# Kernel tuning notes

Measured on AMD Instinct MI355X. Metric: run time of the kernel, lower is better.

Reference implementation:

```python
import jax, jax.numpy as jnp
import numpy as np
from math import factorial

NODES = 40000      # number of nodes
EDGES = 640000     # number of edges (avg degree 16)
MUL = 8            # multiplicity of each irrep in hidden (8x0e+8x1e+8x2e)
NB = 16            # radial basis size (radial_neurons[0])
MAXR = 3.0         # max_radius
NSPECIES = 8
DEG = 16.0         # num_neighbors normalization
R8 = 1.0 / np.sqrt(8.0)

# ---------- real Clebsch-Gordan coefficients (precomputed with numpy) ----------
def _clebsch(j1, m1, j2, m2, j3, m3):
    f = factorial
    if m1 + m2 != m3:
        return 0.0
    pref = ((2*j3+1) * f(j3+j1-j2) * f(j3-j1+j2) * f(j1+j2-j3) / f(j1+j2+j3+1)) ** 0.5
    pref *= (f(j3+m3)*f(j3-m3)*f(j1-m1)*f(j1+m1)*f(j2-m2)*f(j2+m2)) ** 0.5
    lo = max(0, j2-j3-m1, j1-j3+m2)
    hi = min(j1+j2-j3, j1-m1, j2+m2)
    s = 0.0
    for k in range(lo, hi+1):
        s += (-1)**k / (f(k)*f(j1+j2-j3-k)*f(j1-m1-k)*f(j2+m2-k)*f(j3-j2+m1+k)*f(j3-j1-m2+k))
    return pref * s

def _U(l):
    # complex -> real spherical-harmonic change of basis (rows: real m, cols: complex m)
    U = np.zeros((2*l+1, 2*l+1), dtype=complex)
    s2 = 2 ** -0.5
    for m in range(-l, l+1):
        if m > 0:
            U[m+l, m+l] = (-1)**m * s2; U[m+l, -m+l] = s2
        elif m == 0:
            U[l, l] = 1.0
        else:
            U[m+l, m+l] = 1j*s2; U[m+l, -m+l] = -1j*((-1)**m)*s2
    return U

def _real_cg(l1, l2, l3):
    C = np.zeros((2*l1+1, 2*l2+1, 2*l3+1))
    for m1 in range(-l1, l1+1):
        for m2 in range(-l2, l2+1):
            m3 = m1 + m2
            if abs(m3) <= l3:
                C[m1+l1, m2+l2, m3+l3] = _clebsch(l1, m1, l2, m2, l3, m3)
    T = np.einsum('am,bn,co,mno->abc', _U(l1).conj(), _U(l2).conj(), _U(l3), C)
    R = T.imag if np.abs(T.imag).max() > np.abs(T.real).max() else T.real
    return jnp.asarray(R.astype(np.float32))

PATHS = [(0,0,0),(0,1,1),(0,2,2),(1,0,1),(1,1,0),(1,1,1),(1,1,2),
         (1,2,1),(1,2,2),(2,0,2),(2,1,1),(2,1,2),(2,2,0),(2,2,1),(2,2,2)]
CG = {p: _real_cg(*p) for p in PATHS}
NIN = {0: 3.0, 1: 6.0, 2: 6.0}  # fan-in path counts per output l in hidden convs

# ---------- irrep feature layout: [.., 72] = 8x0e | 8x1e | 8x2e ----------
def _split(h):
    lead = h.shape[:-1]
    return (h[..., :MUL],
            h[..., MUL:4*MUL].reshape(lead + (MUL, 3)),
            h[..., 4*MUL:].reshape(lead + (MUL, 5)))

def _merge(s, v, t):
    lead = s.shape[:-1]
    return jnp.concatenate([s, v.reshape(lead + (3*MUL,)), t.reshape(lead + (5*MUL,))], -1)

def _act(h):
    # e3nn Activation: silu on 0e scalars, identity on l>0
    s, v, t = _split(h)
    return _merge(jax.nn.silu(s), v, t)

def _radial(emb, w1, b1, w2, b2):
    return jax.nn.silu(emb @ w1 + b1) @ w2 + b2

def _sh(u):
    # component-normalized real spherical harmonics l=0,1,2 of unit vectors u [E,3]
    x, y, z = u[:, 0], u[:, 1], u[:, 2]
    c15 = np.sqrt(15.0); c5 = np.sqrt(5.0); c3 = np.sqrt(3.0)
    y1 = jnp.stack([y, z, x], -1) * c3
    y2 = jnp.stack([c15*x*y, c15*y*z, 0.5*c5*(3*z*z - 1.0), c15*x*z, 0.5*c15*(x*x - y*y)], -1)
    return jnp.concatenate([jnp.ones_like(x)[:, None], y1, y2], -1)

def _soft_onehot(r):
    # e3nn soft_one_hot_linspace, basis='smooth_finite', cutoff=True
    values = jnp.linspace(0.0, MAXR, NB + 2)[1:-1]
    step = MAXR / (NB + 1)
    d = (r[:, None] - values) / step
    inside = jnp.abs(d) < 1.0
    dd = jnp.where(inside, d, 0.0)
    f = jnp.exp(-1.0 / (1.0 + dd)) * jnp.exp(-1.0 / (1.0 - dd))
    return 1.14136 * np.exp(2.0) * jnp.where(inside, f, 0.0)

def _tp_first(hs, sh, w):
    # uvu TP: 8x0e (x) SH(1x0e+1x1e+1x2e) -> hidden; hs [E,8], sh [E,9], w [E,3,8]
    m_s = w[:, 0] * hs * sh[:, :1]
    m_v = w[:, 1][..., None] * hs[..., None] * sh[:, None, 1:4]
    m_t = w[:, 2][..., None] * hs[..., None] * sh[:, None, 4:9]
    return _merge(m_s, m_v, m_t)

def _tp_uuu(h1, h2, w):
    # depthwise (uuu) CG tensor product hidden (x) hidden -> hidden; w [E,15,8]
    s1, v1, t1 = _split(h1); s2, v2, t2 = _split(h2)
    a = {0: s1[..., None], 1: v1, 2: t1}
    b = {0: s2[..., None], 1: v2, 2: t2}
    out = {0: 0.0, 1: 0.0, 2: 0.0}
    for p, (l1, l2, l3) in enumerate(PATHS):
        out[l3] = out[l3] + w[:, p, :, None] * jnp.einsum('eci,ecj,ijk->eck', a[l1], b[l2], CG[(l1, l2, l3)])
    return _merge(out[0][..., 0] / np.sqrt(NIN[0]), out[1] / np.sqrt(NIN[1]), out[2] / np.sqrt(NIN[2]))

def _lin_hidden(h, lin):
    # irrep-wise linear self-connection, lin [3,8,8]
    s, v, t = _split(h)
    return _merge(s @ lin[0] * R8,
                  jnp.einsum('ncm,cd->ndm', v, lin[1]) * R8,
                  jnp.einsum('ncm,cd->ndm', t, lin[2]) * R8)

def _model(x, edge_index, edge_vec, embed_w, lin0, lin1, lin2, out_w,
           r0_w1, r0_b1, r0_w2, r0_b2, r1_w1, r1_b1, r1_w2, r1_b2,
           r2_w1, r2_b1, r2_w2, r2_b2):
    src, dst = edge_index[0], edge_index[1]
    h = embed_w[x]                                   # [N, 8] scalar node feats
    r = jnp.sqrt(jnp.sum(edge_vec**2, -1) + 1e-12)
    emb = _soft_onehot(r)                            # [E, 16]
    hb_sh = _sh(edge_vec / r[:, None])               # [E, 9]
    rdeg = 1.0 / np.sqrt(DEG)
    # conv 0 + activation
    w = _radial(emb, r0_w1, r0_b1, r0_w2, r0_b2).reshape(-1, 3, MUL)
    m = _tp_first(h[src], hb_sh, w)                  # [E, 72]
    agg = jax.ops.segment_sum(m, dst, num_segments=NODES) * rdeg
    h = _act(agg.at[:, :MUL].add((h @ lin0) * R8))
    hb = _act(m)
    # convs 1..2 + activation
    for (w1, b1, w2, b2, lin) in ((r1_w1, r1_b1, r1_w2, r1_b2, lin1),
                                  (r2_w1, r2_b1, r2_w2, r2_b2, lin2)):
        w = _radial(emb, w1, b1, w2, b2).reshape(-1, 15, MUL)
        m = _tp_uuu(h[src], hb, w)
        agg = jax.ops.segment_sum(m, dst, num_segments=NODES) * rdeg
        h = _act(_lin_hidden(h, lin) + agg)
        hb = _act(m)
    # output FullyConnectedTensorProduct(h, h) -> 8x0e (paths l(x)l->0)
    s, v, t = _split(h)
    i0 = s[:, :, None] * s[:, None, :]
    i1 = jnp.einsum('nim,njm->nij', v, v) / np.sqrt(3.0)
    i2 = jnp.einsum('nim,njm->nij', t, t) / np.sqrt(5.0)
    out = (jnp.einsum('nij,ijk->nk', i0, out_w[0])
           + jnp.einsum('nij,ijk->nk', i1, out_w[1])
           + jnp.einsum('nij,ijk->nk', i2, out_w[2])) / np.sqrt(3.0 * MUL * MUL)
    return out

def setup_inputs() -> dict:
    key = jax.random.key(0)
    ks = jax.random.split(key, 16)
    inp = {}
    inp['x'] = jax.random.randint(ks[0], (NODES,), 0, NSPECIES)
    inp['edge_index'] = jax.random.randint(ks[1], (2, EDGES), 0, NODES)
    inp['edge_vec'] = jax.random.normal(ks[2], (EDGES, 3), dtype=jnp.float32)
    inp['embed_w'] = jax.random.normal(ks[3], (NSPECIES, MUL), dtype=jnp.float32)
    inp['lin0'] = jax.random.normal(ks[4], (MUL, MUL), dtype=jnp.float32)
    inp['lin1'] = jax.random.normal(ks[5], (3, MUL, MUL), dtype=jnp.float32)
    inp['lin2'] = jax.random.normal(ks[6], (3, MUL, MUL), dtype=jnp.float32)
    inp['out_w'] = jax.random.normal(ks[7], (3, MUL, MUL, MUL), dtype=jnp.float32)
    for i, (name, od) in enumerate((('r0', 3*MUL), ('r1', 15*MUL), ('r2', 15*MUL))):
        k1, k2 = jax.random.split(ks[8+i])
        inp[name+'_w1'] = jax.random.normal(k1, (NB, 64), dtype=jnp.float32) / np.sqrt(NB)
        inp[name+'_b1'] = jnp.zeros((64,), dtype=jnp.float32)
        inp[name+'_w2'] = jax.random.normal(k2, (64, od), dtype=jnp.float32) / 8.0
        inp[name+'_b2'] = jnp.zeros((od,), dtype=jnp.float32)
    return inp

def reference(x, edge_index, edge_vec, embed_w, lin0, lin1, lin2, out_w,
              r0_w1, r0_b1, r0_w2, r0_b2, r1_w1, r1_b1, r1_w2, r1_b2,
              r2_w1, r2_b1, r2_w2, r2_b2):
    return _model(x, edge_index, edge_vec, embed_w, lin0, lin1, lin2, out_w,
                  r0_w1, r0_b1, r0_w2, r0_b2, r1_w1, r1_b1, r1_w2, r1_b2,
                  r2_w1, r2_b1, r2_w2, r2_b2)
```

## Files before the change

kernel.cpp:

```cpp
#include <hip/hip_runtime.h>

#define NODES 40000
#define EDGES 640000

typedef float f32x2v __attribute__((ext_vector_type(2)));
typedef float f32x4v __attribute__((ext_vector_type(4)));
typedef short short8v __attribute__((ext_vector_type(8)));

__device__ __forceinline__ float silu_f(float x) { return x / (1.0f + __expf(-x)); }
__device__ __forceinline__ f32x2v mk2(float a, float b) { f32x2v r; r[0] = a; r[1] = b; return r; }

__device__ __forceinline__ void tp_uuu2(const f32x2v* wv,
                                        f32x2v as, const f32x2v* av, const f32x2v* at,
                                        f32x2v bs, const f32x2v* bv, const f32x2v* bt,
                                        f32x2v& ms, f32x2v* mv, f32x2v* mt)
{
    const float CR = 0.70710678f;
    const float K1 = 0.31622777f;
    const float K3 = 0.54772256f;
    const float KA = 0.40824829f;
    const float KB = 0.70710678f;
    const float KC = 0.81649658f;
    const float L4 = 0.63245553f;
    const float G2 = 0.53452248f;
    const float G1 = 0.26726124f;
    const float HH = 0.46291005f;

    f32x2v os = {0.f, 0.f};
    f32x2v ov0 = {0.f, 0.f}, ov1 = {0.f, 0.f}, ov2 = {0.f, 0.f};
    f32x2v ot0 = {0.f, 0.f}, ot1 = {0.f, 0.f}, ot2 = {0.f, 0.f};
    f32x2v ot3 = {0.f, 0.f}, ot4 = {0.f, 0.f};

    os += wv[0] * as * bs;
    ov0 += wv[1] * as * bv[0]; ov1 += wv[1] * as * bv[1]; ov2 += wv[1] * as * bv[2];
    ot0 += wv[2] * as * bt[0]; ot1 += wv[2] * as * bt[1]; ot2 += wv[2] * as * bt[2];
    ot3 += wv[2] * as * bt[3]; ot4 += wv[2] * as * bt[4];
    ov0 += wv[3] * av[0] * bs; ov1 += wv[3] * av[1] * bs; ov2 += wv[3] * av[2] * bs;
    os += wv[4] * (-0.57735027f) * (av[0]*bv[0] + av[1]*bv[1] + av[2]*bv[2]);
    ov0 += wv[5] * CR * (av[1]*bv[2] - av[2]*bv[1]);
    ov1 += wv[5] * CR * (av[2]*bv[0] - av[0]*bv[2]);
    ov2 += wv[5] * CR * (av[0]*bv[1] - av[1]*bv[0]);
    ot0 += wv[6] * CR * (av[2]*bv[0] + av[0]*bv[2]);
    ot1 += wv[6] * CR * (av[0]*bv[1] + av[1]*bv[0]);
    ot2 += wv[6] * 0.40824829f * (2.f*av[1]*bv[1] - av[2]*bv[2] - av[0]*bv[0]);
    ot3 += wv[6] * CR * (av[2]*bv[1] + av[1]*bv[2]);
    ot4 += wv[6] * CR * (av[2]*bv[2] - av[0]*bv[0]);
    ov0 += wv[7] * (-K3*av[1]*bt[1] + K1*av[0]*bt[2] - K3*av[2]*bt[0] + K3*av[0]*bt[4]);
    ov1 += wv[7] * (-2.f*K1*av[1]*bt[2] - K3*av[2]*bt[3] - K3*av[0]*bt[1]);
    ov2 += wv[7] * (-K3*av[1]*bt[3] + K1*av[2]*bt[2] - K3*av[0]*bt[0] - K3*av[2]*bt[4]);
    ot0 += wv[8] * ( KC*av[1]*bt[4] - KA*av[2]*bt[3] + KA*av[0]*bt[1]);
    ot1 += wv[8] * ( KA*av[1]*bt[3] - KB*av[2]*bt[2] - KA*av[0]*bt[0] - KA*av[2]*bt[4]);
    ot2 += wv[8] * ( KB*av[2]*bt[1] - KB*av[0]*bt[3]);
    ot3 += wv[8] * (-KA*av[1]*bt[1] + KB*av[0]*bt[2] + KA*av[2]*bt[0] - KA*av[0]*bt[4]);
    ot4 += wv[8] * (-KC*av[1]*bt[0] + KA*av[2]*bt[1] + KA*av[0]*bt[3]);
    ot0 += wv[9] * at[0] * bs; ot1 += wv[9] * at[1] * bs; ot2 += wv[9] * at[2] * bs;
    ot3 += wv[9] * at[3] * bs; ot4 += wv[9] * at[4] * bs;
    ov0 += wv[10] * (-K3*bv[1]*at[1] + K1*bv[0]*at[2] - K3*bv[2]*at[0] + K3*bv[0]*at[4]);
    ov1 += wv[10] * (-2.f*K1*bv[1]*at[2] - K3*bv[2]*at[3] - K3*bv[0]*at[1]);
    ov2 += wv[10] * (-K3*bv[1]*at[3] + K1*bv[2]*at[2] - K3*bv[0]*at[0] - K3*bv[2]*at[4]);
    ot0 -= wv[11] * ( KC*bv[1]*at[4] - KA*bv[2]*at[3] + KA*bv[0]*at[1]);
    ot1 -= wv[11] * ( KA*bv[1]*at[3] - KB*bv[2]*at[2] - KA*bv[0]*at[0] - KA*bv[2]*at[4]);
    ot2 -= wv[11] * ( KB*bv[2]*at[1] - KB*bv[0]*at[3]);
    ot3 -= wv[11] * (-KA*bv[1]*at[1] + KB*bv[0]*at[2] + KA*bv[2]*at[0] - KA*bv[0]*at[4]);
    ot4 -= wv[11] * (-KC*bv[1]*at[0] + KA*bv[2]*at[1] + KA*bv[0]*at[3]);
    os += wv[12] * 0.44721360f * (at[0]*bt[0] + at[1]*bt[1] + at[2]*bt[2] + at[3]*bt[3] + at[4]*bt[4]);
    ov0 += wv[13] * ( K1*(at[0]*bt[1] - at[1]*bt[0]) + K3*(at[3]*bt[2] - at[2]*bt[3]) + K1*(at[4]*bt[3] - at[3]*bt[4]) );
    ov1 += wv[13] * ( L4*(at[0]*bt[4] - at[4]*bt[0]) + K1*(at[1]*bt[3] - at[3]*bt[1]) );
    ov2 += wv[13] * ( K1*(at[3]*bt[0] - at[0]*bt[3]) + K3*(at[2]*bt[1] - at[1]*bt[2]) + K1*(at[4]*bt[1] - at[1]*bt[4]) );
    ot0 += wv[14] * ( G2*(at[2]*bt[0] + at[0]*bt[2]) - HH*(at[1]*bt[3] + at[3]*bt[1]) );
    ot1 += wv[14] * (-HH*(at[3]*bt[0] + at[0]*bt[3]) + HH*(at[1]*bt[4] + at[4]*bt[1]) - G1*(at[2]*bt[1] + at[1]*bt[2]) );
    ot2 += wv[14] * ( G2*(at[0]*bt[0] + at[4]*bt[4] - at[2]*bt[2]) - G1*(at[1]*bt[1] + at[3]*bt[3]) );
    ot3 += wv[14] * (-HH*(at[1]*bt[0] + at[0]*bt[1]) - HH*(at[3]*bt[4] + at[4]*bt[3]) - G1*(at[2]*bt[3] + at[3]*bt[2]) );
    ot4 += wv[14] * ( G2*(at[2]*bt[4] + at[4]*bt[2]) + HH*(at[1]*bt[1] - at[3]*bt[3]) );

    ms = os * 0.57735027f;
    mv[0] = ov0 * 0.40824829f; mv[1] = ov1 * 0.40824829f; mv[2] = ov2 * 0.40824829f;
    mt[0] = ot0 * 0.40824829f; mt[1] = ot1 * 0.40824829f; mt[2] = ot2 * 0.40824829f;
    mt[3] = ot3 * 0.40824829f; mt[4] = ot4 * 0.40824829f;
}

__global__ void deg_kernel(const int* __restrict__ eidx, int* __restrict__ deg)
{
    int e = blockIdx.x * 256 + threadIdx.x;
    if (e < EDGES) atomicAdd(&deg[eidx[EDGES + e]], 1);
}

__launch_bounds__(1024)
__global__ void scan_kernel(const int* __restrict__ deg, int* __restrict__ off,
                            int* __restrict__ cursor)
{
    __shared__ int part[1024];
    const int t = threadIdx.x;
    const int base = t * 40;
    int v[40];
    if (t < 1000) {
        const int4* p4 = (const int4*)(deg + base);
        #pragma unroll
        for (int i = 0; i < 10; ++i) {
            int4 q = p4[i];
            v[4 * i + 0] = q.x; v[4 * i + 1] = q.y;
            v[4 * i + 2] = q.z; v[4 * i + 3] = q.w;
        }
    } else {
        #pragma unroll
        for (int i = 0; i < 40; ++i) v[i] = 0;
    }
    int loc[40];
    int s = 0;
    #pragma unroll
    for (int i = 0; i < 40; ++i) { loc[i] = s; s += v[i]; }
    part[t] = s;
    __syncthreads();
    for (int d = 1; d < 1024; d <<= 1) {
        int vv = (t >= d) ? part[t - d] : 0;
        __syncthreads();
        part[t] += vv;
        __syncthreads();
    }
    int tb = (t == 0) ? 0 : part[t - 1];
    if (t < 1000) {
        #pragma unroll
        for (int i = 0; i < 40; ++i) {
            off[base + i] = tb + loc[i];
            cursor[base + i] = tb + loc[i];
        }
    }
    if (t == 1023) off[NODES] = part[1023];
}

__global__ void build_kernel(const int* __restrict__ eidx, const float* __restrict__ ev,
                             int* __restrict__ cursor,
                             float* __restrict__ evp, int* __restrict__ srcs)
{
    int e = blockIdx.x * 256 + threadIdx.x;
    if (e < EDGES) {
        int dst = eidx[EDGES + e];
        int p = atomicAdd(&cursor[dst], 1);
        srcs[p] = eidx[e];
        evp[p * 3 + 0] = ev[e * 3 + 0];
        evp[p * 3 + 1] = ev[e * 3 + 1];
        evp[p * 3 + 2] = ev[e * 3 + 2];
    }
}

__launch_bounds__(256, 3)
__global__ void layer0_edge(const float* __restrict__ evp, const int* __restrict__ srcs,
                            const int* __restrict__ xs, const float* __restrict__ embw,
                            const float* __restrict__ w1, const float* __restrict__ b1,
                            const float* __restrict__ w2, const float* __restrict__ b2,
                            float* __restrict__ mbuf)
{
    __shared__ float emb_s[128 * 17];
    __shared__ float hid_s[128 * 68];
    __shared__ float w2t[24 * 68];
    const int tid = threadIdx.x;
    const int e0 = blockIdx.x * 128;

    for (int idx = tid; idx < 64 * 24; idx += 256) {
        int j = idx / 24, o = idx - j * 24;
        w2t[o * 68 + j] = w2[idx];
    }
    for (int idx = tid; idx < 2048; idx += 256) {
        int e = idx >> 4, i = idx & 15;
        const float* ep = evp + (size_t)(e0 + e) * 3;
        float ex = ep[0], ey = ep[1], ez = ep[2];
        float r = sqrtf(ex * ex + ey * ey + ez * ez + 1e-12f);
        float d = r * (17.0f / 3.0f) - (float)(i + 1);
        float f = 0.0f;
        if (fabsf(d) < 1.0f) f = 8.433572869f * __expf(-2.0f / (1.0f - d * d));
        emb_s[e * 17 + i] = f;
    }
    __syncthreads();

    {
        const int egp = tid >> 3;
        const int jb = (tid & 7) * 8;
        float acc2[4][8];
        #pragma unroll
        for (int el = 0; el < 4; ++el)
            #pragma unroll
            for (int k = 0; k < 8; ++k) acc2[el][k] = b1[jb + k];
        #pragma unroll
        for (int i = 0; i < 16; ++i) {
            float4 wa = *(const float4*)&w1[i * 64 + jb];
            float4 wb = *(const float4*)&w1[i * 64 + jb + 4];
            #pragma unroll
            for (int el = 0; el < 4; ++el) {
                float evv = emb_s[(egp * 4 + el) * 17 + i];
                acc2[el][0] += evv * wa.x; acc2[el][1] += evv * wa.y;
                acc2[el][2] += evv * wa.z; acc2[el][3] += evv * wa.w;
                acc2[el][4] += evv * wb.x; acc2[el][5] += evv * wb.y;
                acc2[el][6] += evv * wb.z; acc2[el][7] += evv * wb.w;
            }
        }
        #pragma unroll
        for (int el = 0; el < 4; ++el)
            #pragma unroll
            for (int k = 0; k < 8; ++k)
                hid_s[(egp * 4 + el) * 68 + jb + k] = silu_f(acc2[el][k]);
    }
    __syncthreads();

    const int c = tid & 7, g = (tid >> 3) & 7, wv_ = tid >> 6;
    float wacc[3][4];
    #pragma unroll
    for (int p = 0; p < 3; ++p) {
        float bb = b2[p * 8 + c];
        #pragma unroll
        for (int q = 0; q < 4; ++q) wacc[p][q] = bb;
    }
    for (int jb = 0; jb < 64; jb += 4) {
        float4 h4[4];
        #pragma unroll
        for (int q = 0; q < 4; ++q)
            h4[q] = *(const float4*)&hid_s[(wv_ * 32 + q * 8 + g) * 68 + jb];
        #pragma unroll
        for (int p = 0; p < 3; ++p) {
            float4 w4 = *(const float4*)&w2t[(p * 8 + c) * 68 + jb];
            #pragma unroll
            for (int q = 0; q < 4; ++q)
                wacc[p][q] += h4[q].x * w4.x + h4[q].y * w4.y + h4[q].z * w4.z + h4[q].w * w4.w;
        }
    }

    const int ebase = wv_ * 32 + g;
    const float c3 = 1.7320508f, c15 = 3.8729833f, c5 = 2.2360680f;
    #pragma unroll
    for (int q = 0; q < 4; ++q) {
        const int sl = e0 + ebase + 8 * q;
        const int sn = srcs[sl];
        float hs = embw[xs[sn] * 8 + c];
        const float* ep = evp + (size_t)sl * 3;
        float ex = ep[0], ey = ep[1], ez = ep[2];
        float r = sqrtf(ex * ex + ey * ey + ez * ez + 1e-12f);
        float inv = 1.0f / r;
        float x = ex * inv, y = ey * inv, z = ez * inv;

        float* me = mbuf + (size_t)sl * 72 + c * 9;
        me[0] = wacc[0][q] * hs;
        me[1] = wacc[1][q] * hs * (c3 * y);
        me[2] = wacc[1][q] * hs * (c3 * z);
        me[3] = wacc[1][q] * hs * (c3 * x);
        me[4] = wacc[2][q] * hs * (c15 * x * y);
        me[5] = wacc[2][q] * hs * (c15 * y * z);
        me[6] = wacc[2][q] * hs * (0.5f * c5 * (3.f * z * z - 1.f));
        me[7] = wacc[2][q] * hs * (c15 * x * z);
        me[8] = wacc[2][q] * hs * (0.5f * c15 * (x * x - y * y));
    }
}

__launch_bounds__(256, 3)
__global__ void tp_edge(const float* __restrict__ evp, const int* __restrict__ srcs,
                        const float* __restrict__ h,
                        const float* __restrict__ w1, const float* __restrict__ b1,
                        const float* __restrict__ w2, const float* __restrict__ b2,
                        float* __restrict__ mbuf)
{
    __shared__ float ws_t[120 * 68];
    __shared__ unsigned short hid_s[128 * 64];
    float* emb_s = ws_t;

    const int tid = threadIdx.x;
    const int e0 = blockIdx.x * 128;

    for (int idx = tid; idx < 2048; idx += 256) {
        int e = idx >> 4, i = idx & 15;
        const float* ep = evp + (size_t)(e0 + e) * 3;
        float ex = ep[0], ey = ep[1], ez = ep[2];
        float r = sqrtf(ex * ex + ey * ey + ez * ez + 1e-12f);
        float d = r * (17.0f / 3.0f) - (float)(i + 1);
        float f = 0.0f;
        if (fabsf(d) < 1.0f) f = 8.433572869f * __expf(-2.0f / (1.0f - d * d));
        emb_s[e * 17 + i] = f;
    }
    __syncthreads();

    {
        const int egp = tid >> 3;
        const int jb = (tid & 7) * 8;
        f32x2v acc2[2][8];
        #pragma unroll
        for (int pr = 0; pr < 2; ++pr)
            #pragma unroll
            for (int k = 0; k < 8; ++k) { float bb = b1[jb + k]; acc2[pr][k] = mk2(bb, bb); }
        #pragma unroll
        for (int i = 0; i < 16; ++i) {
            float4 wa = *(const float4*)&w1[i * 64 + jb];
            float4 wb = *(const float4*)&w1[i * 64 + jb + 4];
            #pragma unroll
            for (int pr = 0; pr < 2; ++pr) {
                f32x2v evv = mk2(emb_s[(egp * 4 + 2 * pr) * 17 + i],
                                 emb_s[(egp * 4 + 2 * pr + 1) * 17 + i]);
                acc2[pr][0] += evv * wa.x; acc2[pr][1] += evv * wa.y;
                acc2[pr][2] += evv * wa.z; acc2[pr][3] += evv * wa.w;
                acc2[pr][4] += evv * wb.x; acc2[pr][5] += evv * wb.y;
                acc2[pr][6] += evv * wb.z; acc2[pr][7] += evv * wb.w;
            }
        }
        #pragma unroll
        for (int pr = 0; pr < 2; ++pr) {
            #pragma unroll
            for (int u = 0; u < 2; ++u) {
                unsigned int us[8];
                #pragma unroll
                for (int k = 0; k < 8; ++k) {
                    unsigned int b = __float_as_uint(silu_f(acc2[pr][k][u]));
                    b += 0x7fffu + ((b >> 16) & 1u);
                    us[k] = b >> 16;
                }
                uint4 pk;
                pk.x = us[0] | (us[1] << 16);
                pk.y = us[2] | (us[3] << 16);
                pk.z = us[4] | (us[5] << 16);
                pk.w = us[6] | (us[7] << 16);
                int rr = egp * 4 + 2 * pr + u;
                *(uint4*)&hid_s[rr * 64 + (jb ^ ((rr & 7) << 3))] = pk;
            }
        }
    }
    __syncthreads();

    const int l  = tid & 63;
    const int wq = tid >> 6;
    const int lr = l & 15;
    const int lg = l >> 4;

    short8v bhi[2][2], blo[2][2];
    #pragma unroll
    for (int n2 = 0; n2 < 2; ++n2) {
        int col  = (2 * wq + n2) * 16 + lr;
        int colc = col < 120 ? col : 119;
        #pragma unroll
        for (int ks = 0; ks < 2; ++ks) {
            short8v hv, lv;
            #pragma unroll
            for (int j = 0; j < 8; ++j) {
                int k = ks * 32 + lg * 8 + j;
                float v = w2[k * 120 + colc];
                if (col >= 120) v = 0.0f;
                unsigned bb = __float_as_uint(v);
                unsigned rh = bb + 0x7fffu + ((bb >> 16) & 1u);
                float hf = __uint_as_float((rh >> 16) << 16);
                unsigned bl = __float_as_uint(v - hf);
                bl += 0x7fffu + ((bl >> 16) & 1u);
                hv[j] = (short)(rh >> 16);
                lv[j] = (short)(bl >> 16);
            }
            bhi[n2][ks] = hv;
            blo[n2][ks] = lv;
        }
    }

    const int c = tid & 7, g = (tid >> 3) & 7, wv_ = tid >> 6;
    const int ebh = wv_ * 16 + g;

    #pragma unroll
    for (int half = 0; half < 2; ++half) {
        #pragma unroll
        for (int mm = 0; mm < 4; ++mm) {
            int e  = 64 * half + 16 * mm + lr;
            int sw = (e & 7) << 3;
            short8v a0 = *(const short8v*)&hid_s[e * 64 + ((lg * 8) ^ sw)];
            short8v a1 = *(const short8v*)&hid_s[e * 64 + ((32 + lg * 8) ^ sw)];
            #pragma unroll
            for (int n2 = 0; n2 < 2; ++n2) {
                int col = (2 * wq + n2) * 16 + lr;
                float bias = (col < 120) ? b2[col] : 0.0f;
                f32x4v acc;
                acc[0] = bias; acc[1] = bias; acc[2] = bias; acc[3] = bias;
                acc = __builtin_amdgcn_mfma_f32_16x16x32_bf16(a0, bhi[n2][0], acc, 0, 0, 0);
                acc = __builtin_amdgcn_mfma_f32_16x16x32_bf16(a1, bhi[n2][1], acc, 0, 0, 0);
                acc = __builtin_amdgcn_mfma_f32_16x16x32_bf16(a0, blo[n2][0], acc, 0, 0, 0);
                acc = __builtin_amdgcn_mfma_f32_16x16x32_bf16(a1, blo[n2][1], acc, 0, 0, 0);
                if (col < 120)
                    *(f32x4v*)&ws_t[col * 68 + 16 * mm + lg * 4] = acc;
            }
        }
        __syncthreads();

        {
            const int eA = e0 + 64 * half + ebh;
            const int eB = eA + 8;
            const int snA = srcs[eA], snB = srcs[eB];
            const float* hn0 = h + (size_t)snA * 72 + c * 9;
            const float* hn1 = h + (size_t)snB * 72 + c * 9;
            const float* me0 = mbuf + (size_t)eA * 72 + c * 9;
            const float* me1 = mbuf + (size_t)eB * 72 + c * 9;

            f32x2v as = mk2(hn0[0], hn1[0]);
            f32x2v av[3], at[5], bv[3], bt[5];
            #pragma unroll
            for (int i = 0; i < 3; ++i) av[i] = mk2(hn0[1 + i], hn1[1 + i]);
            #pragma unroll
            for (int i = 0; i < 5; ++i) at[i] = mk2(hn0[4 + i], hn1[4 + i]);
            f32x2v bs = mk2(silu_f(me0[0]), silu_f(me1[0]));
            #pragma unroll
            for (int i = 0; i < 3; ++i) bv[i] = mk2(me0[1 + i], me1[1 + i]);
            #pragma unroll
            for (int i = 0; i < 5; ++i) bt[i] = mk2(me0[4 + i], me1[4 + i]);

            f32x2v wvv[15];
            #pragma unroll
            for (int p = 0; p < 15; ++p)
                wvv[p] = mk2(ws_t[(p * 8 + c) * 68 + ebh],
                             ws_t[(p * 8 + c) * 68 + ebh + 8]);

            f32x2v ms, mv[3], mt[5];
            tp_uuu2(wvv, as, av, at, bs, bv, bt, ms, mv, mt);

            float* mo0 = mbuf + (size_t)eA * 72 + c * 9;
            float* mo1 = mbuf + (size_t)eB * 72 + c * 9;
            mo0[0] = ms[0]; mo1[0] = ms[1];
            #pragma unroll
            for (int i = 0; i < 3; ++i) { mo0[1 + i] = mv[i][0]; mo1[1 + i] = mv[i][1]; }
            #pragma unroll
            for (int i = 0; i < 5; ++i) { mo0[4 + i] = mt[i][0]; mo1[4 + i] = mt[i][1]; }
        }
        if (half == 0) __syncthreads();
    }
}

__global__ void node0(const int* __restrict__ xs, const float* __restrict__ embw,
                      const float* __restrict__ lin0, const float* __restrict__ mbuf,
                      const int* __restrict__ off, float* __restrict__ h)
{
    int idx = blockIdx.x * 256 + threadIdx.x;
    int n = idx >> 3, c = idx & 7;
    int xb = xs[n] * 8;
    float dot = 0.f;
    #pragma unroll
    for (int d = 0; d < 8; ++d) dot += embw[xb + d] * lin0[d * 8 + c];

    float an[9];
    #pragma unroll
    for (int i = 0; i < 9; ++i) an[i] = 0.f;
    const int beg = off[n], end = off[n + 1];
    for (int p = beg; p < end; ++p) {
        const float* me = mbuf + (size_t)p * 72 + c * 9;
        #pragma unroll
        for (int i = 0; i < 9; ++i) an[i] += me[i];
    }

    float* hn = h + (size_t)n * 72 + c * 9;
    hn[0] = silu_f(an[0] * 0.25f + dot * 0.35355339f);
    #pragma unroll
    for (int i = 1; i < 9; ++i) hn[i] = an[i] * 0.25f;
}

__global__ void node12(const float* __restrict__ hin, const float* __restrict__ lin,
                       const float* __restrict__ mbuf, const int* __restrict__ off,
                       float* __restrict__ hout)
{
    int idx = blockIdx.x * 256 + threadIdx.x;
    int n = idx >> 3, d = idx & 7;

    float an[9];
    #pragma unroll
    for (int i = 0; i < 9; ++i) an[i] = 0.f;
    const int beg = off[n], end = off[n + 1];
    for (int p = beg; p < end; ++p) {
        const float* me = mbuf + (size_t)p * 72 + d * 9;
        #pragma unroll
        for (int i = 0; i < 9; ++i) an[i] += me[i];
    }

    const float* hn = hin + (size_t)n * 72;
    float* ho = hout + (size_t)n * 72 + d * 9;

    float s = 0.f;
    #pragma unroll
    for (int c = 0; c < 8; ++c) s += hn[c * 9] * lin[c * 8 + d];
    ho[0] = silu_f(s * 0.35355339f + an[0] * 0.25f);
    #pragma unroll
    for (int i = 0; i < 3; ++i) {
        float v = 0.f;
        #pragma unroll
        for (int c = 0; c < 8; ++c) v += hn[c * 9 + 1 + i] * lin[64 + c * 8 + d];
        ho[1 + i] = v * 0.35355339f + an[1 + i] * 0.25f;
    }
    #pragma unroll
    for (int i = 0; i < 5; ++i) {
        float t = 0.f;
        #pragma unroll
        for (int c = 0; c < 8; ++c) t += hn[c * 9 + 4 + i] * lin[128 + c * 8 + d];
        ho[4 + i] = t * 0.35355339f + an[4 + i] * 0.25f;
    }
}

__global__ void node12_out(const float* __restrict__ hin, const float* __restrict__ lin,
                           const float* __restrict__ mbuf, const int* __restrict__ off,
                           const float* __restrict__ outw, float* __restrict__ out)
{
    __shared__ float hrec[32][72];
    int idx = blockIdx.x * 256 + threadIdx.x;
    int n = idx >> 3, d = idx & 7;
    int nl = threadIdx.x >> 3;

    float an[9];
    #pragma unroll
    for (int i = 0; i < 9; ++i) an[i] = 0.f;
    const int beg = off[n], end = off[n + 1];
    for (int p = beg; p < end; ++p) {
        const float* me = mbuf + (size_t)p * 72 + d * 9;
        #pragma unroll
        for (int i = 0; i < 9; ++i) an[i] += me[i];
    }

    const float* hn = hin + (size_t)n * 72;
    float* ho = &hrec[nl][d * 9];

    float s = 0.f;
    #pragma unroll
    for (int c = 0; c < 8; ++c) s += hn[c * 9] * lin[c * 8 + d];
    ho[0] = silu_f(s * 0.35355339f + an[0] * 0.25f);
    #pragma unroll
    for (int i = 0; i < 3; ++i) {
        float v = 0.f;
        #pragma unroll
        for (int c = 0; c < 8; ++c) v += hn[c * 9 + 1 + i] * lin[64 + c * 8 + d];
        ho[1 + i] = v * 0.35355339f + an[1 + i] * 0.25f;
    }
    #pragma unroll
    for (int i = 0; i < 5; ++i) {
        float t = 0.f;
        #pragma unroll
        for (int c = 0; c < 8; ++c) t += hn[c * 9 + 4 + i] * lin[128 + c * 8 + d];
        ho[4 + i] = t * 0.35355339f + an[4 + i] * 0.25f;
    }
    __syncthreads();

    const float* hr = &hrec[nl][0];
    float sv[8], vv[24], tv[40];
    #pragma unroll
    for (int i = 0; i < 8; ++i) {
        sv[i] = hr[i * 9];
        #pragma unroll
        for (int q = 0; q < 3; ++q) vv[i * 3 + q] = hr[i * 9 + 1 + q];
        #pragma unroll
        for (int q = 0; q < 5; ++q) tv[i * 5 + q] = hr[i * 9 + 4 + q];
    }
    float acc = 0.f;
    #pragma unroll
    for (int i = 0; i < 8; ++i) {
        #pragma unroll
        for (int j = 0; j < 8; ++j) {
            float dv = vv[i*3+0]*vv[j*3+0] + vv[i*3+1]*vv[j*3+1] + vv[i*3+2]*vv[j*3+2];
            float dt = tv[i*5+0]*tv[j*5+0] + tv[i*5+1]*tv[j*5+1] + tv[i*5+2]*tv[j*5+2]
                     + tv[i*5+3]*tv[j*5+3] + tv[i*5+4]*tv[j*5+4];
            int o = (i * 8 + j) * 8 + d;
            acc += sv[i] * sv[j] * outw[o]
                 + dv * 0.57735027f * outw[512 + o]
                 + dt * 0.44721360f * outw[1024 + o];
        }
    }
    out[n * 8 + d] = acc * 0.072168784f;
}

extern "C" void kernel_launch(void* const* d_in, const int* in_sizes, int n_in,
                              void* d_out, int out_size, void* d_ws, size_t ws_size,
                              hipStream_t stream)
{
    const int*   x    = (const int*)  d_in[0];
    const int*   eidx = (const int*)  d_in[1];
    const float* ev   = (const float*)d_in[2];
    const float* embw = (const float*)d_in[3];
    const float* lin0 = (const float*)d_in[4];
    const float* lin1 = (const float*)d_in[5];
    const float* lin2 = (const float*)d_in[6];
    const float* outw = (const float*)d_in[7];
    const float* r0w1 = (const float*)d_in[8];
    const float* r0b1 = (const float*)d_in[9];
    const float* r0w2 = (const float*)d_in[10];
    const float* r0b2 = (const float*)d_in[11];
    const float* r1w1 = (const float*)d_in[12];
    const float* r1b1 = (const float*)d_in[13];
    const float* r1w2 = (const float*)d_in[14];
    const float* r1b2 = (const float*)d_in[15];
    const float* r2w1 = (const float*)d_in[16];
    const float* r2b1 = (const float*)d_in[17];
    const float* r2w2 = (const float*)d_in[18];
    const float* r2b2 = (const float*)d_in[19];

    float* mbuf = (float*)d_ws;
    float* hA   = mbuf + (size_t)EDGES * 72;
    float* hB   = hA + (size_t)NODES * 72;
    float* evp  = hB + (size_t)NODES * 72;
    int*   deg    = (int*)(evp + (size_t)EDGES * 3);
    int*   off    = deg + NODES;
    int*   cursor = off + NODES + 1;
    int*   srcs   = cursor + NODES;

    const int EBI = (EDGES + 255) / 256;
    const int EB  = EDGES / 128;
    const int NBK = NODES * 8 / 256;

    hipMemsetAsync(deg, 0, NODES * sizeof(int), stream);
    deg_kernel<<<EBI, 256, 0, stream>>>(eidx, deg);
    scan_kernel<<<1, 1024, 0, stream>>>(deg, off, cursor);
    build_kernel<<<EBI, 256, 0, stream>>>(eidx, ev, cursor, evp, srcs);

    layer0_edge<<<EB, 256, 0, stream>>>(evp, srcs, x, embw, r0w1, r0b1, r0w2, r0b2, mbuf);
    node0<<<NBK, 256, 0, stream>>>(x, embw, lin0, mbuf, off, hA);

    tp_edge<<<EB, 256, 0, stream>>>(evp, srcs, hA, r1w1, r1b1, r1w2, r1b2, mbuf);
    node12<<<NBK, 256, 0, stream>>>(hA, lin1, mbuf, off, hB);

    tp_edge<<<EB, 256, 0, stream>>>(evp, srcs, hB, r2w1, r2b1, r2w2, r2b2, mbuf);
    node12_out<<<NBK, 256, 0, stream>>>(hB, lin2, mbuf, off, outw, (float*)d_out);
}
```

Before: 680.7 us.

## Fuse segmented atomic aggregation into tp_edge and skip message store in last layer

Packs the destination node into the upper 16 bits of the CSR source array. This lets the tensor-product edge kernel stage each block's messages in shared memory and do a segmented reduction over runs of equal destinations, followed by atomicAdd into a per-node aggregate buffer. The node kernels then read the pre-summed aggregates instead of walking the large edge-message buffer. The last layer no longer writes messages at all. The cost is extra memsets, shared-memory syncs and float atomics, which make the summation order nondeterministic; the packing also relies on node ids fitting in 16 bits.

```diff
diff --git a/kernel.cpp b/kernel.cpp
--- a/kernel.cpp
+++ b/kernel.cpp
@@ -136,7 +136,7 @@
     if (e < EDGES) {
         int dst = eidx[EDGES + e];
         int p = atomicAdd(&cursor[dst], 1);
-        srcs[p] = eidx[e];
+        srcs[p] = (int)(((unsigned)eidx[e]) | ((unsigned)dst << 16));
         evp[p * 3 + 0] = ev[e * 3 + 0];
         evp[p * 3 + 1] = ev[e * 3 + 1];
         evp[p * 3 + 2] = ev[e * 3 + 2];
@@ -228,7 +228,7 @@
     #pragma unroll
     for (int q = 0; q < 4; ++q) {
         const int sl = e0 + ebase + 8 * q;
-        const int sn = srcs[sl];
+        const int sn = (int)((unsigned)srcs[sl] & 0xffffu);
         float hs = embw[xs[sn] * 8 + c];
         const float* ep = evp + (size_t)sl * 3;
         float ex = ep[0], ey = ep[1], ez = ep[2];
@@ -254,10 +254,12 @@
                         const float* __restrict__ h,
                         const float* __restrict__ w1, const float* __restrict__ b1,
                         const float* __restrict__ w2, const float* __restrict__ b2,
-                        float* __restrict__ mbuf)
+                        float* __restrict__ mbuf, float* __restrict__ agg,
+                        const int writeM)
 {
     __shared__ float ws_t[120 * 68];
     __shared__ unsigned short hid_s[128 * 64];
+    __shared__ int dst_s[66];
     float* emb_s = ws_t;
 
     const int tid = threadIdx.x;
@@ -381,7 +383,8 @@
         {
             const int eA = e0 + 64 * half + ebh;
             const int eB = eA + 8;
-            const int snA = srcs[eA], snB = srcs[eB];
+            const unsigned pkA = (unsigned)srcs[eA], pkB = (unsigned)srcs[eB];
+            const int snA = (int)(pkA & 0xffffu), snB = (int)(pkB & 0xffffu);
             const float* hn0 = h + (size_t)snA * 72 + c * 9;
             const float* hn1 = h + (size_t)snB * 72 + c * 9;
             const float* me0 = mbuf + (size_t)eA * 72 + c * 9;
@@ -408,13 +411,54 @@
             f32x2v ms, mv[3], mt[5];
             tp_uuu2(wvv, as, av, at, bs, bv, bt, ms, mv, mt);
 
-            float* mo0 = mbuf + (size_t)eA * 72 + c * 9;
-            float* mo1 = mbuf + (size_t)eB * 72 + c * 9;
-            mo0[0] = ms[0]; mo1[0] = ms[1];
-            #pragma unroll
-            for (int i = 0; i < 3; ++i) { mo0[1 + i] = mv[i][0]; mo1[1 + i] = mv[i][1]; }
-            #pragma unroll
-            for (int i = 0; i < 5; ++i) { mo0[4 + i] = mt[i][0]; mo1[4 + i] = mt[i][1]; }
+            if (writeM) {
+                float* mo0 = mbuf + (size_t)eA * 72 + c * 9;
+                float* mo1 = mbuf + (size_t)eB * 72 + c * 9;
+                mo0[0] = ms[0]; mo1[0] = ms[1];
+                #pragma unroll
+                for (int i = 0; i < 3; ++i) { mo0[1 + i] = mv[i][0]; mo1[1 + i] = mv[i][1]; }
+                #pragma unroll
+                for (int i = 0; i < 5; ++i) { mo0[4 + i] = mt[i][0]; mo1[4 + i] = mt[i][1]; }
+            }
+
+            if (tid <= 64) {
+                int gs = e0 + 64 * half + tid;
+                dst_s[tid] = (gs < EDGES) ? (int)((unsigned)srcs[gs] >> 16) : -1;
+            }
+            __syncthreads();
+
+            float* m_s = ws_t;
+            const int lA = ebh, lB = ebh + 8;
+            m_s[lA * 72 + c * 9] = ms[0]; m_s[lB * 72 + c * 9] = ms[1];
+            #pragma unroll
+            for (int i = 0; i < 3; ++i) {
+                m_s[lA * 72 + c * 9 + 1 + i] = mv[i][0];
+                m_s[lB * 72 + c * 9 + 1 + i] = mv[i][1];
+            }
+            #pragma unroll
+            for (int i = 0; i < 5; ++i) {
+                m_s[lA * 72 + c * 9 + 4 + i] = mt[i][0];
+                m_s[lB * 72 + c * 9 + 4 + i] = mt[i][1];
+            }
+            __syncthreads();
+
+            if (tid < 216) {
+                const int seg  = tid / 72;
+                const int comp = tid - seg * 72;
+                const int p0 = (seg == 0) ? 0  : ((seg == 1) ? 22 : 43);
+                const int p1 = (seg == 0) ? 22 : ((seg == 1) ? 43 : 64);
+                float sum = 0.f;
+                int cur = dst_s[p0];
+                for (int p = p0; p < p1; ++p) {
+                    sum += m_s[p * 72 + comp];
+                    int nxt = dst_s[p + 1];
+                    if (nxt != cur) {
+                        atomicAdd(&agg[(size_t)cur * 72 + comp], sum);
+                        sum = 0.f; cur = nxt;
+                    }
+                }
+                if (cur >= 0) atomicAdd(&agg[(size_t)cur * 72 + comp], sum);
+            }
         }
         if (half == 0) __syncthreads();
     }
@@ -448,21 +492,14 @@
 }
 
 __global__ void node12(const float* __restrict__ hin, const float* __restrict__ lin,
-                       const float* __restrict__ mbuf, const int* __restrict__ off,
-                       float* __restrict__ hout)
+                       const float* __restrict__ agg, float* __restrict__ hout)
 {
     int idx = blockIdx.x * 256 + threadIdx.x;
     int n = idx >> 3, d = idx & 7;
 
     float an[9];
     #pragma unroll
-    for (int i = 0; i < 9; ++i) an[i] = 0.f;
-    const int beg = off[n], end = off[n + 1];
-    for (int p = beg; p < end; ++p) {
-        const float* me = mbuf + (size_t)p * 72 + d * 9;
-        #pragma unroll
-        for (int i = 0; i < 9; ++i) an[i] += me[i];
-    }
+    for (int i = 0; i < 9; ++i) an[i] = agg[(size_t)n * 72 + d * 9 + i];
 
     const float* hn = hin + (size_t)n * 72;
     float* ho = hout + (size_t)n * 72 + d * 9;
@@ -488,7 +525,7 @@
 }
 
 __global__ void node12_out(const float* __restrict__ hin, const float* __restrict__ lin,
-                           const float* __restrict__ mbuf, const int* __restrict__ off,
+                           const float* __restrict__ agg,
                            const float* __restrict__ outw, float* __restrict__ out)
 {
     __shared__ float hrec[32][72];
@@ -498,13 +535,7 @@
 
     float an[9];
     #pragma unroll
-    for (int i = 0; i < 9; ++i) an[i] = 0.f;
-    const int beg = off[n], end = off[n + 1];
-    for (int p = beg; p < end; ++p) {
-        const float* me = mbuf + (size_t)p * 72 + d * 9;
-        #pragma unroll
-        for (int i = 0; i < 9; ++i) an[i] += me[i];
-    }
+    for (int i = 0; i < 9; ++i) an[i] = agg[(size_t)n * 72 + d * 9 + i];
 
     const float* hn = hin + (size_t)n * 72;
     float* ho = &hrec[nl][d * 9];
@@ -593,8 +624,10 @@
     const int EBI = (EDGES + 255) / 256;
     const int EB  = EDGES / 128;
     const int NBK = NODES * 8 / 256;
+    const size_t HBYTES = (size_t)NODES * 72 * sizeof(float);
 
     hipMemsetAsync(deg, 0, NODES * sizeof(int), stream);
+    hipMemsetAsync(hB, 0, HBYTES, stream);
     deg_kernel<<<EBI, 256, 0, stream>>>(eidx, deg);
     scan_kernel<<<1, 1024, 0, stream>>>(deg, off, cursor);
     build_kernel<<<EBI, 256, 0, stream>>>(eidx, ev, cursor, evp, srcs);
@@ -602,9 +635,10 @@
     layer0_edge<<<EB, 256, 0, stream>>>(evp, srcs, x, embw, r0w1, r0b1, r0w2, r0b2, mbuf);
     node0<<<NBK, 256, 0, stream>>>(x, embw, lin0, mbuf, off, hA);
 
-    tp_edge<<<EB, 256, 0, stream>>>(evp, srcs, hA, r1w1, r1b1, r1w2, r1b2, mbuf);
-    node12<<<NBK, 256, 0, stream>>>(hA, lin1, mbuf, off, hB);
-
-    tp_edge<<<EB, 256, 0, stream>>>(evp, srcs, hB, r2w1, r2b1, r2w2, r2b2, mbuf);
-    node12_out<<<NBK, 256, 0, stream>>>(hB, lin2, mbuf, off, outw, (float*)d_out);
-}
+    tp_edge<<<EB, 256, 0, stream>>>(evp, srcs, hA, r1w1, r1b1, r1w2, r1b2, mbuf, hB, 1);
+    node12<<<NBK, 256, 0, stream>>>(hA, lin1, hB, hB);
+
+    hipMemsetAsync(hA, 0, HBYTES, stream);
+    tp_edge<<<EB, 256, 0, stream>>>(evp, srcs, hB, r2w1, r2b1, r2w2, r2b2, mbuf, hA, 0);
+    node12_out<<<NBK, 256, 0, stream>>>(hB, lin2, hA, outw, (float*)d_out);
+}
```

After: 672.7 us. Within noise of the previous version (-1.2%).
